# Optimization experiments

Hardware: AMD Instinct MI355X
Metric: run time of the kernel (lower is better)

Reference implementation:

```python
import jax, jax.numpy as jnp
import numpy as np

D_MODEL = 512
D_STATE = 64
D_CONV = 4
EXPAND = 2
D_INNER = EXPAND * D_MODEL          # 1024
DT_RANK = (D_MODEL + 15) // 16      # 32 (ceil(d_model/16), standard Mamba)
B, L = 2, 1024
EPS = 1e-6


def setup_inputs() -> dict:
    key = jax.random.key(0)
    ks = jax.random.split(key, 12)
    s = 0.02
    p = {}
    p["x"] = jax.random.normal(ks[0], (B, L, D_MODEL), jnp.float32)
    # shared _Mamba params (share_dir=True)
    p["W_in"] = jax.random.normal(ks[1], (2 * D_INNER, D_MODEL), jnp.float32) * s
    p["conv_w"] = jax.random.normal(ks[2], (D_INNER, 1, D_CONV), jnp.float32) * s
    p["conv_b"] = jnp.zeros((D_INNER,), jnp.float32)
    p["W_xproj"] = jax.random.normal(ks[3], (DT_RANK + 2 * D_STATE, D_INNER), jnp.float32) * s
    p["W_dt"] = jax.random.normal(ks[4], (D_INNER, DT_RANK), jnp.float32) * s
    p["b_dt"] = jax.random.uniform(ks[5], (D_INNER,), jnp.float32, -4.0, -2.0)  # small dt after softplus
    p["A_log"] = jnp.log(jnp.broadcast_to(jnp.arange(1, D_STATE + 1, dtype=jnp.float32), (D_INNER, D_STATE)))
    p["Dskip"] = jnp.ones((D_INNER,), jnp.float32)
    p["W_out"] = jax.random.normal(ks[6], (D_MODEL, D_INNER), jnp.float32) * s
    # block params
    p["norm_in_w"] = jnp.ones((D_MODEL,), jnp.float32)
    p["fuse_W"] = jax.random.normal(ks[7], (2 * D_MODEL, 2 * D_MODEL), jnp.float32) * s
    p["fuse_b"] = jnp.zeros((2 * D_MODEL,), jnp.float32)
    p["ff_W1"] = jax.random.normal(ks[8], (4 * D_MODEL, D_MODEL), jnp.float32) * s
    p["ff_W2"] = jax.random.normal(ks[9], (D_MODEL, 4 * D_MODEL), jnp.float32) * s
    p["norm_out_w"] = jnp.ones((D_MODEL,), jnp.float32)
    return p


def _rmsnorm(x, w):
    x32 = x.astype(jnp.float32)
    var = jnp.mean(x32 * x32, axis=-1, keepdims=True)
    return (w * (x32 * jax.lax.rsqrt(var + EPS))).astype(x.dtype)


def _mamba(h, W_in, conv_w, conv_b, W_xproj, W_dt, b_dt, A_log, Dskip, W_out):
    # h: [B, L, D_MODEL]
    xz = jnp.einsum('bld,ed->ble', h, W_in)           # [B,L,2*D_INNER]
    u, z = jnp.split(xz, 2, axis=-1)
    # depthwise causal conv over time
    uc = jnp.transpose(u, (0, 2, 1))                  # [B,D_INNER,L]
    uc = jax.lax.conv_general_dilated(uc, conv_w, (1,), [(D_CONV - 1, 0)],
                                      feature_group_count=D_INNER)
    u = jax.nn.silu(jnp.transpose(uc, (0, 2, 1)) + conv_b)  # [B,L,D_INNER]
    x_dbl = jnp.einsum('bld,ed->ble', u, W_xproj)     # [B,L,DT_RANK+2N]
    dt = jax.nn.softplus(jnp.einsum('blr,dr->bld', x_dbl[..., :DT_RANK], W_dt) + b_dt)  # [B,L,D_INNER]
    Bm = x_dbl[..., DT_RANK:DT_RANK + D_STATE]        # [B,L,N]
    Cm = x_dbl[..., DT_RANK + D_STATE:]               # [B,L,N]
    A = -jnp.exp(A_log)                               # [D_INNER,N]

    def step(s, inp):
        dt_t, B_t, C_t, u_t = inp                     # [B,Din],[B,N],[B,N],[B,Din]
        dA = jnp.exp(dt_t[..., None] * A)             # [B,Din,N]
        s = s * dA + (dt_t * u_t)[..., None] * B_t[:, None, :]
        y_t = jnp.einsum('bdn,bn->bd', s, C_t)
        return s, y_t

    s0 = jnp.zeros((h.shape[0], D_INNER, D_STATE), h.dtype)
    xs = (jnp.moveaxis(dt, 1, 0), jnp.moveaxis(Bm, 1, 0),
          jnp.moveaxis(Cm, 1, 0), jnp.moveaxis(u, 1, 0))
    _, ys = jax.lax.scan(step, s0, xs)                # [L,B,D_INNER]
    y = jnp.moveaxis(ys, 0, 1) + u * Dskip
    return jnp.einsum('bld,ed->ble', y * jax.nn.silu(z), W_out)


def reference(x, W_in, conv_w, conv_b, W_xproj, W_dt, b_dt, A_log, Dskip, W_out,
              norm_in_w, fuse_W, fuse_b, ff_W1, ff_W2, norm_out_w):
    h = _rmsnorm(x, norm_in_w)
    mam = lambda t: _mamba(t, W_in, conv_w, conv_b, W_xproj, W_dt, b_dt, A_log, Dskip, W_out)
    hf = mam(h)
    hb = jnp.flip(mam(jnp.flip(h, axis=1)), axis=1)   # shared params (share_dir=True)
    hcat = jnp.concatenate([hf, hb], axis=-1)         # [B,L,2D]
    uv = jnp.einsum('ble,fe->blf', hcat, fuse_W) + fuse_b
    ug, vg = jnp.split(uv, 2, axis=-1)
    h = ug * jax.nn.sigmoid(vg)                        # GLU fuse
    ff = jnp.einsum('bld,fd->blf', jax.nn.silu(h), ff_W1)
    ff = jnp.einsum('blf,df->bld', jax.nn.silu(ff), ff_W2)
    y = x + ff                                         # dropout=0 (eval)
    return _rmsnorm(y, norm_out_w)
```

## Files before the change

kernel.cpp:

```cpp
#include <hip/hip_runtime.h>
#include <math.h>

#define L_SEQ 1024
#define NC 32
#define CL 32

typedef unsigned short ushort_t;
typedef __attribute__((ext_vector_type(8))) short bf16x8_t;
typedef __attribute__((ext_vector_type(4))) float f32x4_t;
typedef __attribute__((ext_vector_type(2))) float f32x2_t;

__device__ __forceinline__ float sigmoidf_(float x){ return 1.f/(1.f+__expf(-x)); }
__device__ __forceinline__ float siluf_(float x){ return x*sigmoidf_(x); }
__device__ __forceinline__ float softplusf_(float x){ return (x>20.f)?x:log1pf(__expf(x)); }
__device__ __forceinline__ ushort_t f2bf(float f){
  union { float f; unsigned u; } a; a.f = f;
  unsigned u = a.u;
  unsigned r = (u + 0x7fffu + ((u >> 16) & 1u)) >> 16;
  return (ushort_t)r;
}
__device__ __forceinline__ float bf2f(ushort_t v){
  union { unsigned u; float f; } a; a.u = ((unsigned)v) << 16; return a.f;
}
__device__ __forceinline__ ushort_t f2h(float f){
  union { _Float16 h; ushort_t u; } c; c.h = (_Float16)f; return c.u;
}
__device__ __forceinline__ float h2f(ushort_t u){
  union { ushort_t u; _Float16 h; } c; c.u = u; return (float)c.h;
}

__global__ __launch_bounds__(256) void cast_all_weights(
    ushort_t* __restrict__ dst,
    const float* __restrict__ W_in, const float* __restrict__ W_xproj,
    const float* __restrict__ W_dt, const float* __restrict__ W_out,
    const float* __restrict__ fuse_W, const float* __restrict__ ff_W1,
    const float* __restrict__ ff_W2)
{
  int i = blockIdx.x*256 + threadIdx.x;
  if (i >= 4947968) return;
  float v;
  if (i < 1048576) v = W_in[i];
  else if (i < 1245184) { int j = i-1048576; v = (j < 163840) ? W_xproj[j] : 0.f; }
  else if (i < 1277952) v = W_dt[i-1245184];
  else if (i < 1802240) v = W_out[i-1277952];
  else if (i < 2850816) {
    int j2 = i-1802240;
    int r_new = j2 >> 10, col = j2 & 1023;
    int jj = r_new >> 1;
    int old_r = (r_new & 1) ? (512 + jj) : jj;
    v = fuse_W[(size_t)old_r*1024 + col];
  }
  else if (i < 3899392) v = ff_W1[i-2850816];
  else v = ff_W2[i-3899392];
  dst[i] = f2bf(v);
}

__global__ __launch_bounds__(256) void rmsnorm_kernel(
    float* __restrict__ outf, ushort_t* __restrict__ outb,
    const float* __restrict__ in, const float* __restrict__ res,
    const float* __restrict__ res2, const float* __restrict__ w)
{
  int row = blockIdx.x, tid = threadIdx.x;
  size_t base = (size_t)row*512;
  float v0 = in[base+tid], v1 = in[base+tid+256];
  if (res)  { v0 += res[base+tid];  v1 += res[base+tid+256]; }
  if (res2) { v0 += res2[base+tid]; v1 += res2[base+tid+256]; }
  float ss = v0*v0 + v1*v1;
  #pragma unroll
  for (int off=32; off>0; off>>=1) ss += __shfl_down(ss, off, 64);
  __shared__ float red[4];
  int wv = tid>>6, ln = tid&63;
  if (ln==0) red[wv]=ss;
  __syncthreads();
  float tot = red[0]+red[1]+red[2]+red[3];
  float sc = rsqrtf(tot*(1.f/512.f) + 1e-6f);
  float o0 = w[tid]*v0*sc, o1 = w[tid+256]*v1*sc;
  if (outb) { outb[base+tid] = f2bf(o0); outb[base+tid+256] = f2bf(o1); }
  else      { outf[base+tid] = o0;       outf[base+tid+256] = o1; }
}

template<int TM, int TN>
__global__ __launch_bounds__(256) void mfma_gemm(
    const ushort_t* __restrict__ A, int lda,
    const ushort_t* __restrict__ W, int ldw,
    float* __restrict__ Cf, ushort_t* __restrict__ Cb, int ldc,
    int N, int K, const float* __restrict__ bias, int act, int dsplit,
    int kz_cstride)
{
  constexpr int BM = 32*TM, BN = 32*TN;
  constexpr int NSEG = (BM + BN) / 16;
  __shared__ ushort_t As[2][BM*32];
  __shared__ ushort_t Bs[2][BN*32];
  const int tid = threadIdx.x;
  const int wid = tid >> 6, lane = tid & 63;
  const int wm = (wid & 1) * (16*TM);
  const int wn = (wid >> 1) * (16*TN);
  const int row0 = blockIdx.y * BM;
  const int col0 = blockIdx.x * BN;
  const int zz = blockIdx.z;
  const int kbase = zz * K;
  const int qd = lane >> 4, lr = lane & 15;
  const int seg_row = lane >> 2;
  const int seg_swz = (seg_row & 3) ^ ((seg_row >> 2) & 3);
  const int seg_col = ((lane & 3) ^ seg_swz) * 8;
  const int rd_swz  = (lr & 3) ^ ((lr >> 2) & 3);
  const int rd_off  = (qd ^ rd_swz) * 8;

  f32x4_t acc[TM][TN];
  #pragma unroll
  for (int i=0;i<TM;++i)
    #pragma unroll
    for (int j=0;j<TN;++j) acc[i][j] = (f32x4_t)(0.f);

  auto STAGE = [&](int buf, int k0) {
    #pragma unroll
    for (int ss = 0; ss < NSEG/4; ++ss) {
      int s = wid + ss*4;
      bool isA = (s < BM/16);
      int r = isA ? s*16 : (s - BM/16)*16;
      const ushort_t* gp = isA
          ? (A + (size_t)(row0 + r + seg_row)*lda + kbase + k0 + seg_col)
          : (W + (size_t)(col0 + r + seg_row)*ldw + kbase + k0 + seg_col);
      ushort_t* lp = (isA ? As[buf] : Bs[buf]) + r*32;
      __builtin_amdgcn_global_load_lds(
          (const __attribute__((address_space(1))) void*)gp,
          (__attribute__((address_space(3))) void*)lp, 16, 0, 0);
    }
  };

  const int nt = K >> 5;
  STAGE(0, 0);
  __syncthreads();
  for (int t = 0; t < nt; ++t) {
    const int cur = t & 1;
    if (t + 1 < nt) STAGE(cur ^ 1, (t + 1) << 5);
    bf16x8_t af[TM], bfv[TN];
    #pragma unroll
    for (int mi=0; mi<TM; ++mi)
      af[mi] = *(const bf16x8_t*)(As[cur] + (wm + mi*16 + lr)*32 + rd_off);
    #pragma unroll
    for (int ni=0; ni<TN; ++ni)
      bfv[ni] = *(const bf16x8_t*)(Bs[cur] + (wn + ni*16 + lr)*32 + rd_off);
    #pragma unroll
    for (int mi=0; mi<TM; ++mi)
      #pragma unroll
      for (int ni=0; ni<TN; ++ni)
        acc[mi][ni] = __builtin_amdgcn_mfma_f32_16x16x32_bf16(af[mi], bfv[ni], acc[mi][ni], 0, 0, 0);
    __syncthreads();
  }

  #pragma unroll
  for (int ni=0; ni<TN; ++ni) {
    int col = col0 + wn + ni*16 + lr;
    if (col >= N) continue;
    int bcol = (act==3) ? (((col & 1) ? 512 : 0) + (col >> 1)) : col;
    float bv = bias ? bias[bcol] : 0.f;
    #pragma unroll
    for (int mi=0; mi<TM; ++mi) {
      #pragma unroll
      for (int r=0; r<4; ++r) {
        int row = row0 + wm + mi*16 + qd*4 + r;
        float v = acc[mi][ni][r] + bv;
        if (act == 3) {
          float vp = __shfl_xor(v, 1, 64);
          if ((col & 1) == 0) {
            float hv = v * sigmoidf_(vp);
            Cb[(size_t)row*512 + (col >> 1)] = f2bf(siluf_(hv));
          }
          continue;
        }
        if (act == 1) v = softplusf_(v);
        else if (act == 2) v = siluf_(v);
        size_t off;
        if (dsplit && row >= 2048) off = (size_t)(row-2048)*ldc + 512 + col;
        else                       off = (size_t)row*ldc + col;
        off += (size_t)zz * kz_cstride;
        if (Cf) Cf[off] = v;
        if (Cb) Cb[off] = f2bf(v);
      }
    }
  }
}

__global__ __launch_bounds__(256) void conv_silu_kernel(
    ushort_t* __restrict__ ubf, const ushort_t* __restrict__ xzb,
    const float* __restrict__ conv_w, const float* __restrict__ conv_b)
{
  size_t gid = (size_t)blockIdx.x*256 + threadIdx.x;
  int d   = gid & 1023;
  int l   = (gid >> 10) & 1023;
  int b   = (gid >> 20) & 1;
  int dir = (int)(gid >> 21);
  const float4 wv = ((const float4*)conv_w)[d];
  const float wk[4] = {wv.x, wv.y, wv.z, wv.w};
  const ushort_t* xp = xzb + (size_t)b*L_SEQ*2048 + d;
  float acc = conv_b[d];
  if (dir == 0) {
    #pragma unroll
    for (int k=0;k<4;++k){ int ll=l-3+k; if(ll>=0) acc += bf2f(xp[(size_t)ll*2048])*wk[k]; }
  } else {
    #pragma unroll
    for (int k=0;k<4;++k){ int ll=l+3-k; if(ll<L_SEQ) acc += bf2f(xp[(size_t)ll*2048])*wk[k]; }
  }
  size_t oidx = (size_t)dir*2097152 + ((size_t)b*L_SEQ + l)*1024 + d;
  ubf[oidx] = f2bf(siluf_(acc));
}

#define DTB_M 16
__global__ __launch_bounds__(256) void dt_prep_kernel(
    const float* __restrict__ xdblf, const float* __restrict__ W_dt,
    const float* __restrict__ b_dt, const ushort_t* __restrict__ ub,
    ushort_t* __restrict__ rb, ushort_t* __restrict__ dtub)
{
  __shared__ float wsm[32*256];
  __shared__ float xr[DTB_M*32];
  int tid = threadIdx.x;
  int d0 = blockIdx.x << 8;
  int m0 = blockIdx.y * DTB_M;
  {
    const float4* src = (const float4*)(W_dt + ((size_t)(d0 + tid))*32);
    #pragma unroll
    for (int k4=0;k4<8;++k4) {
      float4 v = src[k4];
      wsm[(k4*4+0)*256 + tid] = v.x;
      wsm[(k4*4+1)*256 + tid] = v.y;
      wsm[(k4*4+2)*256 + tid] = v.z;
      wsm[(k4*4+3)*256 + tid] = v.w;
    }
  }
  if (tid < DTB_M*8) {
    int li = tid >> 3, fo = (tid & 7) << 2;
    *(float4*)(xr + li*32 + fo) = *(const float4*)(xdblf + (size_t)(m0+li)*160 + fo);
  }
  __syncthreads();
  int d = d0 + tid;
  float w[32];
  #pragma unroll
  for (int k=0;k<32;++k) w[k] = wsm[k*256 + tid];
  float bias = b_dt[d];
  #pragma unroll 1
  for (int i=0;i<DTB_M;++i) {
    const float4* xrow = (const float4*)(xr + i*32);
    float acc = bias;
    #pragma unroll
    for (int k4=0;k4<8;++k4) {
      float4 xv = xrow[k4];
      acc += w[4*k4+0]*xv.x + w[4*k4+1]*xv.y + w[4*k4+2]*xv.z + w[4*k4+3]*xv.w;
    }
    float dt = softplusf_(acc);
    size_t off = (size_t)(m0+i)*1024 + d;
    float uu = bf2f(ub[off]);
    rb[off]   = f2h(__expf(-dt));
    dtub[off] = f2bf(dt*uu);
  }
}


__global__ __launch_bounds__(256) void scan_pass1(
    const ushort_t* __restrict__ rb, const ushort_t* __restrict__ dtub,
    const float* __restrict__ xdbl,
    float* __restrict__ prch, ushort_t* __restrict__ qbuf)
{
  __shared__ float bst[CL*64];
  int tid = threadIdx.x;
  int dblk = blockIdx.x, c = blockIdx.y, sd = blockIdx.z;
  int b = sd>>1, dir = sd&1;
  int d = (dblk<<8) + tid;
  size_t dbo = (size_t)dir*2097152 + (size_t)b*1048576;
  const float* xd = xdbl + (size_t)dir*327680 + (size_t)b*163840;
  int l0c = c*CL;
  #pragma unroll
  for (int e = tid; e < CL*16; e += 256) {
    int li = e >> 4, fo = (e & 15) << 2;
    int l = dir ? (L_SEQ-1-(l0c+li)) : (l0c+li);
    *(float4*)(bst + li*64 + fo) = *(const float4*)(xd + (size_t)l*160 + 32 + fo);
  }
  __syncthreads();
  f32x2_t s2[32];
  #pragma unroll
  for (int p=0;p<32;++p) s2[p]=(f32x2_t)(0.f);
  float pr = 1.f;
  int l0 = dir ? (L_SEQ-1-l0c) : l0c;
  int lstep = dir ? -1024 : 1024;
  const ushort_t* rpl = rb   + dbo + (size_t)l0*1024 + d;
  const ushort_t* dpl = dtub + dbo + (size_t)l0*1024 + d;
  float rv_n = h2f(*rpl);
  float du_n = bf2f(*dpl);
  #pragma unroll 1
  for (int i=0;i<CL;++i) {
    float rv = rv_n, du = du_n;
    if (i+1 < CL) {
      rpl += lstep; dpl += lstep;
      rv_n = h2f(*rpl); du_n = bf2f(*dpl);
    }
    const f32x2_t* B2 = (const f32x2_t*)(bst + i*64);
    pr *= rv;
    float r2 = rv*rv, r4 = r2*r2;
    f32x2_t c01 = {rv, r2};
    f32x2_t c23 = {r2*rv, r4};
    f32x2_t r44 = {r4, r4};
    f32x2_t du2 = {du, du};
    #pragma unroll
    for (int jj=0;jj<16;++jj) {
      s2[2*jj+0] = s2[2*jj+0]*c01 + du2*B2[2*jj+0];
      s2[2*jj+1] = s2[2*jj+1]*c23 + du2*B2[2*jj+1];
      c01 *= r44; c23 *= r44;
    }
  }
  prch[((size_t)sd*NC + c)*1024 + d] = pr;
  ushort_t* qp = qbuf + ((size_t)(sd*NC + c)*64)*1024 + d;
  #pragma unroll
  for (int n=0;n<64;++n) qp[(size_t)n*1024] = f2bf(s2[n>>1][n&1]);
}

__global__ __launch_bounds__(256) void scan_pass2(
    const float* __restrict__ prch, ushort_t* __restrict__ qbuf)
{
  int gid = blockIdx.x*256 + threadIdx.x;
  int d  = gid & 1023;
  int n  = (gid >> 10) & 63;
  int sd = gid >> 16;
  float np1 = (float)(n+1);
  float s = 0.f;
  #pragma unroll 1
  for (int c=0;c<NC;++c) {
    size_t qidx = ((size_t)(sd*NC+c)*64 + n)*1024 + d;
    float qv = bf2f(qbuf[qidx]);
    float pr = prch[((size_t)sd*NC+c)*1024 + d];
    float P  = __expf(np1 * __logf(pr));
    qbuf[qidx] = f2bf(s);
    s = s*P + qv;
  }
}

__global__ __launch_bounds__(256) void scan_pass3(
    const ushort_t* __restrict__ rb, const ushort_t* __restrict__ dtub,
    const ushort_t* __restrict__ ub, const float* __restrict__ xdbl,
    const ushort_t* __restrict__ qbuf, const ushort_t* __restrict__ xzb,
    const float* __restrict__ Dskip, ushort_t* __restrict__ ycb)
{
  __shared__ float bcst[CL*128];
  int tid = threadIdx.x;
  int dblk = blockIdx.x, c = blockIdx.y, sd = blockIdx.z;
  int b = sd>>1, dir = sd&1;
  int d = (dblk<<8) + tid;
  size_t dbo = (size_t)dir*2097152 + (size_t)b*1048576;
  const float* xd = xdbl + (size_t)dir*327680 + (size_t)b*163840;
  int l0c = c*CL;
  #pragma unroll
  for (int e = tid; e < CL*32; e += 256) {
    int li = e >> 5, fo = (e & 31) << 2;
    int l = dir ? (L_SEQ-1-(l0c+li)) : (l0c+li);
    *(float4*)(bcst + li*128 + fo) = *(const float4*)(xd + (size_t)l*160 + 32 + fo);
  }
  f32x2_t s2[32];
  const ushort_t* qp = qbuf + ((size_t)(sd*NC + c)*64)*1024 + d;
  #pragma unroll
  for (int n=0;n<64;++n) s2[n>>1][n&1] = bf2f(qp[(size_t)n*1024]);
  float Dv = Dskip[d];
  int l0 = dir ? (L_SEQ-1-l0c) : l0c;
  int lstep = dir ? -1024 : 1024;
  int zstep = dir ? -2048 : 2048;
  const ushort_t* rpl = rb   + dbo + (size_t)l0*1024 + d;
  const ushort_t* dpl = dtub + dbo + (size_t)l0*1024 + d;
  const ushort_t* upl = ub   + dbo + (size_t)l0*1024 + d;
  const ushort_t* zpl = xzb + ((size_t)b*L_SEQ + l0)*2048 + 1024 + d;
  ushort_t*       ypl = ycb + dbo + (size_t)l0*1024 + d;
  float rv_n = h2f(*rpl);
  float du_n = bf2f(*dpl);
  float uv_n = bf2f(*upl);
  float zv_n = bf2f(*zpl);
  __syncthreads();
  #pragma unroll 1
  for (int i=0;i<CL;++i) {
    float rv = rv_n, du = du_n, uvv = uv_n, zv = zv_n;
    if (i+1 < CL) {
      rpl += lstep; dpl += lstep; upl += lstep; zpl += zstep;
      rv_n = h2f(*rpl); du_n = bf2f(*dpl); uv_n = bf2f(*upl); zv_n = bf2f(*zpl);
    }
    const f32x2_t* B2 = (const f32x2_t*)(bcst + i*128);
    const f32x2_t* C2 = (const f32x2_t*)(bcst + i*128 + 64);
    float r2 = rv*rv, r4 = r2*r2;
    f32x2_t c01 = {rv, r2};
    f32x2_t c23 = {r2*rv, r4};
    f32x2_t r44 = {r4, r4};
    f32x2_t du2 = {du, du};
    f32x2_t y01 = (f32x2_t)(0.f), y23 = (f32x2_t)(0.f);
    #pragma unroll
    for (int jj=0;jj<16;++jj) {
      s2[2*jj+0] = s2[2*jj+0]*c01 + du2*B2[2*jj+0];
      y01 = y01 + s2[2*jj+0]*C2[2*jj+0];
      s2[2*jj+1] = s2[2*jj+1]*c23 + du2*B2[2*jj+1];
      y23 = y23 + s2[2*jj+1]*C2[2*jj+1];
      c01 *= r44; c23 *= r44;
    }
    float yv = (y01[0]+y01[1])+(y23[0]+y23[1]) + uvv*Dv;
    *ypl = f2bf(yv * siluf_(zv));
    ypl += lstep;
  }
}

extern "C" void kernel_launch(void* const* d_in, const int* in_sizes, int n_in,
                              void* d_out, int out_size, void* d_ws, size_t ws_size,
                              hipStream_t stream) {
  const float* x        = (const float*)d_in[0];
  const float* W_in     = (const float*)d_in[1];
  const float* conv_w   = (const float*)d_in[2];
  const float* conv_b   = (const float*)d_in[3];
  const float* W_xproj  = (const float*)d_in[4];
  const float* W_dt     = (const float*)d_in[5];
  const float* b_dt     = (const float*)d_in[6];
  const float* Dskip    = (const float*)d_in[8];
  const float* W_out    = (const float*)d_in[9];
  const float* norm_in_w  = (const float*)d_in[10];
  const float* fuse_W   = (const float*)d_in[11];
  const float* fuse_b   = (const float*)d_in[12];
  const float* ff_W1    = (const float*)d_in[13];
  const float* ff_W2    = (const float*)d_in[14];
  const float* norm_out_w = (const float*)d_in[15];
  float* out = (float*)d_out;

  float* ws = (float*)d_ws;
  ushort_t* xzb   = (ushort_t*)(ws + 0);
  ushort_t* ubf   = (ushort_t*)(ws + 2097152);
  float*    xdblf = ws + 4194304;
  ushort_t* rb    = (ushort_t*)(ws + 5177344);
  ushort_t* dtub  = (ushort_t*)(ws + 7274496);
  float*    prch  = ws + 9371648;
  ushort_t* qbuf  = (ushort_t*)(ws + 9633792);
  ushort_t* h_bf  = (ushort_t*)(ws + 9633792);
  ushort_t* wb    = (ushort_t*)(ws + 18022400);
  ushort_t* W_in_bf  = wb;
  ushort_t* W_xp_bf  = wb + 1048576;
  ushort_t* W_out_bf = wb + 1277952;
  ushort_t* fuseW_bf = wb + 1802240;
  ushort_t* ffW1_bf  = wb + 2850816;
  ushort_t* ffW2_bf  = wb + 3899392;
  ushort_t* ycb  = ubf;
  ushort_t* hfhb = (ushort_t*)(ws + 5177344);
  ushort_t* h2s  = (ushort_t*)(ws + 2097152);
  ushort_t* ff1s = (ushort_t*)(ws + 9633792);
  float*    ff2p = ws + 7274496;

  cast_all_weights<<<19328, 256, 0, stream>>>(wb, W_in, W_xproj, W_dt, W_out,
                                              fuse_W, ff_W1, ff_W2);
  rmsnorm_kernel<<<2048, 256, 0, stream>>>(nullptr, h_bf, x, nullptr, nullptr, norm_in_w);
  mfma_gemm<2,4><<<dim3(16,32), 256, 0, stream>>>(h_bf,512, W_in_bf,512,
      nullptr, xzb, 2048, 2048,512, nullptr,0,0, 0);
  conv_silu_kernel<<<16384, 256, 0, stream>>>(ubf, xzb, conv_w, conv_b);
  mfma_gemm<2,2><<<dim3(3,64), 256, 0, stream>>>(ubf,1024, W_xp_bf,1024,
      xdblf, nullptr, 160, 160,1024, nullptr,0,0, 0);
  dt_prep_kernel<<<dim3(4,256), 256, 0, stream>>>(xdblf, W_dt, b_dt, ubf, rb, dtub);
  scan_pass1<<<dim3(4,NC,4), 256, 0, stream>>>(rb, dtub, xdblf, prch, qbuf);
  scan_pass2<<<1024, 256, 0, stream>>>(prch, qbuf);
  scan_pass3<<<dim3(4,NC,4), 256, 0, stream>>>(rb, dtub, ubf, xdblf, qbuf, xzb, Dskip, ycb);
  mfma_gemm<2,2><<<dim3(8,64), 256, 0, stream>>>(ycb,1024, W_out_bf,1024,
      nullptr, hfhb, 1024, 512,1024, nullptr,0,1, 0);
  mfma_gemm<2,2><<<dim3(16,32), 256, 0, stream>>>(hfhb,1024, fuseW_bf,1024,
      nullptr, h2s, 512, 1024,1024, fuse_b,3,0, 0);
  mfma_gemm<2,4><<<dim3(16,32), 256, 0, stream>>>(h2s,512, ffW1_bf,512,
      nullptr, ff1s, 2048, 2048,512, nullptr,2,0, 0);
  mfma_gemm<2,2><<<dim3(8,32,2), 256, 0, stream>>>(ff1s,2048, ffW2_bf,2048,
      ff2p, nullptr, 512, 512,1024, nullptr,0,0, 1048576);
  rmsnorm_kernel<<<2048, 256, 0, stream>>>(out, nullptr, ff2p, x, ff2p + 1048576, norm_out_w);
}
```

Before: 333.3 us.

## Triple-buffer GEMM LDS staging with vmcnt waits and fuse weight cast with input RMSNorm

The MFMA GEMM goes from double-buffered to triple-buffered LDS staging. Loads are issued two K-tiles ahead, and explicit s_waitcnt vmcnt plus a raw s_barrier replace __syncthreads, so global-to-LDS copies overlap more with compute. The weight cast kernel and the input RMSNorm are merged into one launch to save a kernel launch. The unconditional prefetch in the last two iterations reads past the K range of each tile, which risks out-of-bounds reads, and the larger LDS use may lower occupancy.

```diff
diff --git a/kernel.cpp b/kernel.cpp
--- a/kernel.cpp
+++ b/kernel.cpp
@@ -28,43 +28,51 @@
 __device__ __forceinline__ float h2f(ushort_t u){
   union { ushort_t u; _Float16 h; } c; c.u = u; return (float)c.h;
 }
-
-__global__ __launch_bounds__(256) void cast_all_weights(
+template<int N> __device__ __forceinline__ void waitcnt_vm() {
+  if constexpr (N==2)      asm volatile("s_waitcnt vmcnt(2)" ::: "memory");
+  else if constexpr (N==3) asm volatile("s_waitcnt vmcnt(3)" ::: "memory");
+  else if constexpr (N==4) asm volatile("s_waitcnt vmcnt(4)" ::: "memory");
+  else if constexpr (N==6) asm volatile("s_waitcnt vmcnt(6)" ::: "memory");
+  __builtin_amdgcn_sched_barrier(0);
+}
+__device__ __forceinline__ void block_barrier() {
+  __builtin_amdgcn_s_barrier();
+  __builtin_amdgcn_sched_barrier(0);
+}
+
+__global__ __launch_bounds__(256) void prep_kernel(
     ushort_t* __restrict__ dst,
     const float* __restrict__ W_in, const float* __restrict__ W_xproj,
     const float* __restrict__ W_dt, const float* __restrict__ W_out,
     const float* __restrict__ fuse_W, const float* __restrict__ ff_W1,
-    const float* __restrict__ ff_W2)
-{
-  int i = blockIdx.x*256 + threadIdx.x;
-  if (i >= 4947968) return;
-  float v;
-  if (i < 1048576) v = W_in[i];
-  else if (i < 1245184) { int j = i-1048576; v = (j < 163840) ? W_xproj[j] : 0.f; }
-  else if (i < 1277952) v = W_dt[i-1245184];
-  else if (i < 1802240) v = W_out[i-1277952];
-  else if (i < 2850816) {
-    int j2 = i-1802240;
-    int r_new = j2 >> 10, col = j2 & 1023;
-    int jj = r_new >> 1;
-    int old_r = (r_new & 1) ? (512 + jj) : jj;
-    v = fuse_W[(size_t)old_r*1024 + col];
-  }
-  else if (i < 3899392) v = ff_W1[i-2850816];
-  else v = ff_W2[i-3899392];
-  dst[i] = f2bf(v);
-}
-
-__global__ __launch_bounds__(256) void rmsnorm_kernel(
-    float* __restrict__ outf, ushort_t* __restrict__ outb,
-    const float* __restrict__ in, const float* __restrict__ res,
-    const float* __restrict__ res2, const float* __restrict__ w)
-{
-  int row = blockIdx.x, tid = threadIdx.x;
+    const float* __restrict__ ff_W2,
+    const float* __restrict__ x, const float* __restrict__ norm_in_w,
+    ushort_t* __restrict__ h_bf)
+{
+  int blk = blockIdx.x, tid = threadIdx.x;
+  if (blk < 19328) {
+    int i = blk*256 + tid;
+    if (i >= 4947968) return;
+    float v;
+    if (i < 1048576) v = W_in[i];
+    else if (i < 1245184) { int j = i-1048576; v = (j < 163840) ? W_xproj[j] : 0.f; }
+    else if (i < 1277952) v = W_dt[i-1245184];
+    else if (i < 1802240) v = W_out[i-1277952];
+    else if (i < 2850816) {
+      int j2 = i-1802240;
+      int r_new = j2 >> 10, col = j2 & 1023;
+      int jj = r_new >> 1;
+      int old_r = (r_new & 1) ? (512 + jj) : jj;
+      v = fuse_W[(size_t)old_r*1024 + col];
+    }
+    else if (i < 3899392) v = ff_W1[i-2850816];
+    else v = ff_W2[i-3899392];
+    dst[i] = f2bf(v);
+    return;
+  }
+  int row = blk - 19328;
   size_t base = (size_t)row*512;
-  float v0 = in[base+tid], v1 = in[base+tid+256];
-  if (res)  { v0 += res[base+tid];  v1 += res[base+tid+256]; }
-  if (res2) { v0 += res2[base+tid]; v1 += res2[base+tid+256]; }
+  float v0 = x[base+tid], v1 = x[base+tid+256];
   float ss = v0*v0 + v1*v1;
   #pragma unroll
   for (int off=32; off>0; off>>=1) ss += __shfl_down(ss, off, 64);
@@ -74,9 +82,31 @@
   __syncthreads();
   float tot = red[0]+red[1]+red[2]+red[3];
   float sc = rsqrtf(tot*(1.f/512.f) + 1e-6f);
-  float o0 = w[tid]*v0*sc, o1 = w[tid+256]*v1*sc;
-  if (outb) { outb[base+tid] = f2bf(o0); outb[base+tid+256] = f2bf(o1); }
-  else      { outf[base+tid] = o0;       outf[base+tid+256] = o1; }
+  h_bf[base+tid]     = f2bf(norm_in_w[tid]*v0*sc);
+  h_bf[base+tid+256] = f2bf(norm_in_w[tid+256]*v1*sc);
+}
+
+__global__ __launch_bounds__(256) void rmsnorm_kernel(
+    float* __restrict__ outf,
+    const float* __restrict__ in, const float* __restrict__ res,
+    const float* __restrict__ res2, const float* __restrict__ w)
+{
+  int row = blockIdx.x, tid = threadIdx.x;
+  size_t base = (size_t)row*512;
+  float v0 = in[base+tid], v1 = in[base+tid+256];
+  v0 += res[base+tid];  v1 += res[base+tid+256];
+  v0 += res2[base+tid]; v1 += res2[base+tid+256];
+  float ss = v0*v0 + v1*v1;
+  #pragma unroll
+  for (int off=32; off>0; off>>=1) ss += __shfl_down(ss, off, 64);
+  __shared__ float red[4];
+  int wv = tid>>6, ln = tid&63;
+  if (ln==0) red[wv]=ss;
+  __syncthreads();
+  float tot = red[0]+red[1]+red[2]+red[3];
+  float sc = rsqrtf(tot*(1.f/512.f) + 1e-6f);
+  outf[base+tid]     = w[tid]*v0*sc;
+  outf[base+tid+256] = w[tid+256]*v1*sc;
 }
 
 template<int TM, int TN>
@@ -89,8 +119,9 @@
 {
   constexpr int BM = 32*TM, BN = 32*TN;
   constexpr int NSEG = (BM + BN) / 16;
-  __shared__ ushort_t As[2][BM*32];
-  __shared__ ushort_t Bs[2][BN*32];
+  constexpr int LPS  = NSEG/4;
+  __shared__ ushort_t As[3][BM*32];
+  __shared__ ushort_t Bs[3][BN*32];
   const int tid = threadIdx.x;
   const int wid = tid >> 6, lane = tid & 63;
   const int wm = (wid & 1) * (16*TM);
@@ -114,7 +145,7 @@
 
   auto STAGE = [&](int buf, int k0) {
     #pragma unroll
-    for (int ss = 0; ss < NSEG/4; ++ss) {
+    for (int ss = 0; ss < LPS; ++ss) {
       int s = wid + ss*4;
       bool isA = (s < BM/16);
       int r = isA ? s*16 : (s - BM/16)*16;
@@ -130,23 +161,28 @@
 
   const int nt = K >> 5;
   STAGE(0, 0);
-  __syncthreads();
+  STAGE(1, 32);
+  waitcnt_vm<LPS>();
+  block_barrier();
   for (int t = 0; t < nt; ++t) {
-    const int cur = t & 1;
-    if (t + 1 < nt) STAGE(cur ^ 1, (t + 1) << 5);
+    STAGE((t+2)%3, (t+2) << 5);
+    waitcnt_vm<2*LPS>();
+    block_barrier();
+    const ushort_t* Ab = As[t%3];
+    const ushort_t* Bb = Bs[t%3];
     bf16x8_t af[TM], bfv[TN];
     #pragma unroll
     for (int mi=0; mi<TM; ++mi)
-      af[mi] = *(const bf16x8_t*)(As[cur] + (wm + mi*16 + lr)*32 + rd_off);
+      af[mi] = *(const bf16x8_t*)(Ab + (wm + mi*16 + lr)*32 + rd_off);
     #pragma unroll
     for (int ni=0; ni<TN; ++ni)
-      bfv[ni] = *(const bf16x8_t*)(Bs[cur] + (wn + ni*16 + lr)*32 + rd_off);
+      bfv[ni] = *(const bf16x8_t*)(Bb + (wn + ni*16 + lr)*32 + rd_off);
     #pragma unroll
     for (int mi=0; mi<TM; ++mi)
       #pragma unroll
       for (int ni=0; ni<TN; ++ni)
         acc[mi][ni] = __builtin_amdgcn_mfma_f32_16x16x32_bf16(af[mi], bfv[ni], acc[mi][ni], 0, 0, 0);
-    __syncthreads();
+    block_barrier();
   }
 
   #pragma unroll
@@ -442,9 +478,8 @@
   ushort_t* ff1s = (ushort_t*)(ws + 9633792);
   float*    ff2p = ws + 7274496;
 
-  cast_all_weights<<<19328, 256, 0, stream>>>(wb, W_in, W_xproj, W_dt, W_out,
-                                              fuse_W, ff_W1, ff_W2);
-  rmsnorm_kernel<<<2048, 256, 0, stream>>>(nullptr, h_bf, x, nullptr, nullptr, norm_in_w);
+  prep_kernel<<<21376, 256, 0, stream>>>(wb, W_in, W_xproj, W_dt, W_out,
+      fuse_W, ff_W1, ff_W2, x, norm_in_w, h_bf);
   mfma_gemm<2,4><<<dim3(16,32), 256, 0, stream>>>(h_bf,512, W_in_bf,512,
       nullptr, xzb, 2048, 2048,512, nullptr,0,0, 0);
   conv_silu_kernel<<<16384, 256, 0, stream>>>(ubf, xzb, conv_w, conv_b);
@@ -462,5 +497,5 @@
       nullptr, ff1s, 2048, 2048,512, nullptr,2,0, 0);
   mfma_gemm<2,2><<<dim3(8,32,2), 256, 0, stream>>>(ff1s,2048, ffW2_bf,2048,
       ff2p, nullptr, 512, 512,1024, nullptr,0,0, 1048576);
-  rmsnorm_kernel<<<2048, 256, 0, stream>>>(out, nullptr, ff2p, x, ff2p + 1048576, norm_out_w);
-}
+  rmsnorm_kernel<<<2048, 256, 0, stream>>>(out, ff2p, x, ff2p + 1048576, norm_out_w);
+}
```

Result: slower. 345.4 us (+3.6%).
